# Kernel optimization log

Measured on AMD Instinct MI355X. Metric: run time of the kernel, lower is better.

## Reference

```python
import jax, jax.numpy as jnp
import numpy as np
from jax import lax

B0, H0, W0, C0, NH0 = 8, 128, 128, 192, 6
SPLIT = (8, 16)
BN_EPS = 1e-5


def setup_inputs() -> dict:
    key = jax.random.key(0)
    ks = jax.random.split(key, 32)
    r = lambda i, shape, s=0.02: jax.random.normal(ks[i], shape, dtype=jnp.float32) * s
    C, C8 = C0, C0 // 8
    L = H0 * W0
    return dict(
        x=jax.random.normal(ks[0], (B0, L, C), dtype=jnp.float32),
        w_qkv=r(1, (C, 3 * C)), b_qkv=r(2, (3 * C,)),
        w_dw1=r(3, (C, 1, 3, 3), 0.1), b_dw1=r(4, (C,)),
        g_bn1=1.0 + r(5, (C,)), be_bn1=r(6, (C,)),
        w_si1=r(7, (C8, C), 0.05), b_si1=r(8, (C8,)),
        g_si=1.0 + r(9, (C8,)), be_si=r(10, (C8,)),
        w_si2=r(11, (1, C8), 0.05), b_si2=r(12, (1,)),
        w_ci1=r(13, (C8, C), 0.05), b_ci1=r(14, (C8,)),
        g_ci=1.0 + r(15, (C8,)), be_ci=r(16, (C8,)),
        w_ci2=r(17, (C, C8), 0.05), b_ci2=r(18, (C,)),
        w_dw2=r(19, (C, 1, 3, 3), 0.1), b_dw2=r(20, (C,)),
        g_bn2=1.0 + r(21, (C,)), be_bn2=r(22, (C,)),
        w_proj=r(23, (C, C)), b_proj=r(24, (C,)),
        H=H0, W=W0,
    )


def _bn(x, g, b):  # eval-mode BatchNorm2d, running_mean=0, running_var=1, NCHW
    return x * (g / jnp.sqrt(1.0 + BN_EPS))[:, None, None] + b[:, None, None]


def _gelu(x):
    return jax.nn.gelu(x, approximate=False)  # torch nn.GELU default (erf)


def _dwconv3x3(x, w, b):  # x:(B,C,H,W), w:(C,1,3,3) depthwise
    y = lax.conv_general_dilated(x, w, (1, 1), 'SAME',
                                 feature_group_count=x.shape[1],
                                 dimension_numbers=('NCHW', 'OIHW', 'NCHW'))
    return y + b[:, None, None]


def _c1x1(x, w, b):  # 1x1 conv, w:(O,C)
    return jnp.einsum('bchw,oc->bohw', x, w) + b[:, None, None]


def _win_attn(q, k, v, H, W, Hs, Ws, nh):
    # q,k,v: (B, H*W, Cb). qkv1==qkv2==qkv3 in the source (same Linear on same x),
    # so attn1+attn2+attn3 == 3*attn1 and v1+v2+v3 == 3*v1 (faithful math).
    B, L, Cb = q.shape
    hd = Cb // nh
    scale = hd ** (-0.5)
    T = Hs * Ws

    def to_win(t):  # (B,L,Cb) -> (nW, nh, T, hd)
        t = t.reshape(B, H // Hs, Hs, W // Ws, Ws, Cb)
        t = t.transpose(0, 1, 3, 2, 4, 5).reshape(-1, T, nh, hd)
        return t.transpose(0, 2, 1, 3)

    qw, kw, vw = to_win(q), to_win(k), to_win(v)
    attn = jnp.einsum('wntd,wnsd->wnts', qw, kw) * (3.0 * scale)
    attn = jax.nn.softmax(attn, axis=-1)
    out = jnp.einsum('wnts,wnsd->wntd', attn, 3.0 * vw)  # (nW, nh, T, hd)
    out = out.transpose(0, 2, 1, 3).reshape(-1, T, Cb)
    out = out.reshape(B, H // Hs, W // Ws, Hs, Ws, Cb)
    out = out.transpose(0, 1, 3, 2, 4, 5).reshape(B, H, W, Cb)
    return out


def _forward(x, w_qkv, b_qkv, w_dw1, b_dw1, g_bn1, be_bn1,
             w_si1, b_si1, g_si, be_si, w_si2, b_si2,
             w_ci1, b_ci1, g_ci, be_ci, w_ci2, b_ci2,
             w_dw2, b_dw2, g_bn2, be_bn2, w_proj, b_proj, H, W):
    B, L, C = x.shape
    Ch = C // 2
    nh = NH0 // 2

    qkv = (x @ w_qkv + b_qkv).reshape(B, L, 3, C).transpose(2, 0, 1, 3)  # (3,B,L,C)
    mx = max(SPLIT)
    pad_b = (mx - H % mx) % mx
    pad_r = (mx - W % mx) % mx
    qi = qkv.reshape(3 * B, H, W, C)
    qi = jnp.pad(qi, ((0, 0), (0, pad_b), (0, pad_r), (0, 0)))
    _H, _W = H + pad_b, W + pad_r
    qkv = qi.reshape(3, B, _H * _W, C)
    q, k, v = qkv[0], qkv[1], qkv[2]

    fu1 = _win_attn(q[..., :Ch], k[..., :Ch], v[..., :Ch], _H, _W, SPLIT[0], SPLIT[1], nh)
    fu2 = _win_attn(q[..., Ch:], k[..., Ch:], v[..., Ch:], _H, _W, SPLIT[1], SPLIT[0], nh)
    fu = jnp.concatenate([fu1[:, :H, :W, :].reshape(B, L, Ch),
                          fu2[:, :H, :W, :].reshape(B, L, Ch)], axis=-1)

    # NOTE: the source does x.reshape(B,C,L) (a raw reshape, NOT a transpose) -- replicated.
    x_img = x.reshape(B, C, H, W)
    conv_x1 = _gelu(_bn(_dwconv3x3(x_img, w_dw1, b_dw1), g_bn1, be_bn1))

    s = _c1x1(conv_x1, w_si1, b_si1)
    s = _c1x1(_gelu(_bn(s, g_si, be_si)), w_si2, b_si2)   # (B,1,H,W)
    spatial_map = s.reshape(B, L, 1)

    c = conv_x1.mean(axis=(2, 3), keepdims=True)           # AdaptiveAvgPool2d(1)
    c = _c1x1(c, w_ci1, b_ci1)
    c = _c1x1(_gelu(_bn(c, g_ci, be_ci)), w_ci2, b_ci2)    # (B,C,1,1)
    channel_map = c.reshape(B, 1, C)

    fu = fu + fu * jax.nn.sigmoid(spatial_map)
    fu_img = jnp.swapaxes(fu, -2, -1).reshape(B, C, H, W)
    fu_img = _gelu(_bn(_dwconv3x3(fu_img, w_dw2, b_dw2), g_bn2, be_bn2))
    fu = fu_img.transpose(0, 2, 3, 1).reshape(B, L, C)
    fu = fu + fu * jax.nn.sigmoid(channel_map)
    return fu @ w_proj + b_proj


def reference(x, w_qkv, b_qkv, w_dw1, b_dw1, g_bn1, be_bn1,
              w_si1, b_si1, g_si, be_si, w_si2, b_si2,
              w_ci1, b_ci1, g_ci, be_ci, w_ci2, b_ci2,
              w_dw2, b_dw2, g_bn2, be_bn2, w_proj, b_proj, H, W):
    return _forward(x, w_qkv, b_qkv, w_dw1, b_dw1, g_bn1, be_bn1,
                    w_si1, b_si1, g_si, be_si, w_si2, b_si2,
                    w_ci1, b_ci1, g_ci, be_ci, w_ci2, b_ci2,
                    w_dw2, b_dw2, g_bn2, be_bn2, w_proj, b_proj, H, W)
```

## Files before the change

### kernel.cpp

```cpp
#include <hip/hip_runtime.h>

#define Bn 8
#define Hn 128
#define Wn 128
#define Cn 192
#define Ln (Hn*Wn)
#define Mn (Bn*Ln)
#define FUn ((size_t)Mn*Cn)
#define BANKn ((size_t)Mn*96)
#define BN_RSQ 0.9999950000374997f

typedef unsigned short ushort_t;
typedef __attribute__((ext_vector_type(8))) short short8;
typedef __attribute__((ext_vector_type(4))) float f32x4;
typedef __attribute__((ext_vector_type(4))) unsigned int uint4v;

static __device__ __forceinline__ float gelu_f(float x) {
    return 0.5f * x * (1.0f + erff(x * 0.7071067811865475f));
}
static __device__ __forceinline__ float gate1p(float x) {
    return 1.0f + 1.0f / (1.0f + __expf(-x));
}
static __device__ __forceinline__ unsigned short f2bf(float f) {
    unsigned u = __float_as_uint(f);
    return (unsigned short)((u + 0x7FFFu + ((u >> 16) & 1u)) >> 16);
}
static __device__ __forceinline__ unsigned int pk2(float lo, float hi) {
    return (unsigned int)f2bf(lo) | ((unsigned int)f2bf(hi) << 16);
}
static __device__ __forceinline__ float bf2f(ushort_t u) {
    return __uint_as_float((unsigned)u << 16);
}

__global__ __launch_bounds__(256) void qkv_mfma(const ushort_t* __restrict__ Ab,
        const float* __restrict__ Bw, const float* __restrict__ bias,
        ushort_t* __restrict__ Qp, ushort_t* __restrict__ Kp,
        ushort_t* __restrict__ Vp)
{
    __shared__ __align__(16) ushort_t As[128 * 64];
    __shared__ __align__(16) ushort_t Bs[96 * 64];
    const int m0 = blockIdx.y * 128;
    const int n0g = blockIdx.x * 96;
    const int part = n0g / 192;
    const int coln = n0g - part * 192;
    ushort_t* dst = part == 0 ? Qp : (part == 1 ? Kp : Vp);
    ushort_t* bptr = dst + (coln ? BANKn : 0);
    const int tid = threadIdx.x;
    const int lane = tid & 63;
    const int wrow = (tid >> 6) * 32;
    const int r0 = lane >> 4, cl = lane & 15;
    f32x4 acc[2][6] = {};

    for (int ks = 0; ks < 3; ++ks) {
        const int k0 = ks * 64;
        if (ks) __syncthreads();
        #pragma unroll
        for (int i = 0; i < 2; ++i) {
            int s = tid + i * 256;
            int row = s >> 2, q = s & 3;
            const ushort_t* src = Ab + (size_t)(m0 + row) * 192 + k0 + q * 16;
            uint4 u0 = *(const uint4*)(src);
            uint4 u1 = *(const uint4*)(src + 8);
            int r7 = row & 7;
            *(uint4*)&As[row * 64 + (((q * 2) ^ r7) * 8)] = u0;
            *(uint4*)&As[row * 64 + (((q * 2 + 1) ^ r7) * 8)] = u1;
        }
        #pragma unroll
        for (int i = 0; i < 3; ++i) {
            int f = tid + i * 256;
            int col = f % 96, kslot = f / 96;
            uint4v wv;
            #pragma unroll
            for (int e2 = 0; e2 < 4; ++e2) {
                float lo = Bw[(size_t)(k0 + kslot * 8 + 2 * e2)     * 576 + n0g + col];
                float hi = Bw[(size_t)(k0 + kslot * 8 + 2 * e2 + 1) * 576 + n0g + col];
                wv[e2] = pk2(lo, hi);
            }
            *(uint4v*)&Bs[col * 64 + ((kslot ^ (col & 7)) * 8)] = wv;
        }
        __syncthreads();
        #pragma unroll
        for (int kk = 0; kk < 2; ++kk) {
            int kslot = kk * 4 + r0;
            int ra0 = wrow + cl, ra1 = wrow + 16 + cl;
            short8 a0 = *(const short8*)&As[ra0 * 64 + ((kslot ^ (ra0 & 7)) * 8)];
            short8 a1 = *(const short8*)&As[ra1 * 64 + ((kslot ^ (ra1 & 7)) * 8)];
            #pragma unroll
            for (int n = 0; n < 6; ++n) {
                int col = n * 16 + cl;
                short8 bn = *(const short8*)&Bs[col * 64 + ((kslot ^ (col & 7)) * 8)];
                acc[0][n] = __builtin_amdgcn_mfma_f32_16x16x32_bf16(a0, bn, acc[0][n], 0, 0, 0);
                acc[1][n] = __builtin_amdgcn_mfma_f32_16x16x32_bf16(a1, bn, acc[1][n], 0, 0, 0);
            }
        }
    }
    float bv[6];
    #pragma unroll
    for (int n = 0; n < 6; ++n) bv[n] = bias[n0g + n * 16 + cl];
    #pragma unroll
    for (int m = 0; m < 2; ++m) {
        #pragma unroll
        for (int j = 0; j < 4; ++j) {
            int row = m0 + wrow + m * 16 + r0 * 4 + j;
            int b = row >> 14, l = row & 16383;
            int h = l >> 7, w = l & 127;
            int win, t;
            if (coln == 0) { win = (h >> 3) * 8 + (w >> 4);  t = (h & 7) * 16 + (w & 15); }
            else           { win = (h >> 4) * 16 + (w >> 3); t = (h & 15) * 8 + (w & 7); }
            size_t wb3 = (size_t)(b * 128 + win) * 3;
            #pragma unroll
            for (int n = 0; n < 6; ++n) {
                int col96 = n * 16 + cl;
                int head = col96 >> 5, ch = col96 & 31;
                size_t off = (wb3 + head) * 4096 +
                             (part == 2 ? ch * 128 + t : t * 32 + ch);
                bptr[off] = f2bf(acc[m][n][j] + bv[n]);
            }
        }
    }
}

__global__ __launch_bounds__(256) void proj_mfma(const ushort_t* __restrict__ Ab,
        const float* __restrict__ Bw, const float* __restrict__ bias,
        float* __restrict__ Cout)
{
    __shared__ __align__(16) ushort_t As[128 * 64];
    __shared__ __align__(16) ushort_t Bs[96 * 64];
    const int m0 = blockIdx.x * 128;
    const int n0 = blockIdx.y * 96;
    const int tid = threadIdx.x;
    const int lane = tid & 63;
    const int wrow = (tid >> 6) * 32;
    const int r0 = lane >> 4, cl = lane & 15;
    f32x4 acc[2][6] = {};

    for (int ks = 0; ks < 3; ++ks) {
        const int k0 = ks * 64;
        if (ks) __syncthreads();
        #pragma unroll
        for (int i = 0; i < 2; ++i) {
            int s = tid + i * 256;
            int row = s >> 2, q = s & 3;
            const ushort_t* src = Ab + (size_t)(m0 + row) * 192 + k0 + q * 16;
            uint4 u0 = *(const uint4*)(src);
            uint4 u1 = *(const uint4*)(src + 8);
            int r7 = row & 7;
            *(uint4*)&As[row * 64 + (((q * 2) ^ r7) * 8)] = u0;
            *(uint4*)&As[row * 64 + (((q * 2 + 1) ^ r7) * 8)] = u1;
        }
        #pragma unroll
        for (int i = 0; i < 3; ++i) {
            int f = tid + i * 256;
            int col = f % 96, kslot = f / 96;
            uint4v wv;
            #pragma unroll
            for (int e2 = 0; e2 < 4; ++e2) {
                float lo = Bw[(size_t)(k0 + kslot * 8 + 2 * e2)     * 192 + n0 + col];
                float hi = Bw[(size_t)(k0 + kslot * 8 + 2 * e2 + 1) * 192 + n0 + col];
                wv[e2] = pk2(lo, hi);
            }
            *(uint4v*)&Bs[col * 64 + ((kslot ^ (col & 7)) * 8)] = wv;
        }
        __syncthreads();
        #pragma unroll
        for (int kk = 0; kk < 2; ++kk) {
            int kslot = kk * 4 + r0;
            int ra0 = wrow + cl, ra1 = wrow + 16 + cl;
            short8 a0 = *(const short8*)&As[ra0 * 64 + ((kslot ^ (ra0 & 7)) * 8)];
            short8 a1 = *(const short8*)&As[ra1 * 64 + ((kslot ^ (ra1 & 7)) * 8)];
            #pragma unroll
            for (int n = 0; n < 6; ++n) {
                int col = n * 16 + cl;
                short8 bn = *(const short8*)&Bs[col * 64 + ((kslot ^ (col & 7)) * 8)];
                acc[0][n] = __builtin_amdgcn_mfma_f32_16x16x32_bf16(a0, bn, acc[0][n], 0, 0, 0);
                acc[1][n] = __builtin_amdgcn_mfma_f32_16x16x32_bf16(a1, bn, acc[1][n], 0, 0, 0);
            }
        }
    }
    #pragma unroll
    for (int m = 0; m < 2; ++m) {
        #pragma unroll
        for (int n = 0; n < 6; ++n) {
            int col = n0 + n * 16 + cl;
            float bv = bias[col];
            #pragma unroll
            for (int j = 0; j < 4; ++j) {
                int row = m0 + wrow + m * 16 + r0 * 4 + j;
                Cout[(size_t)row * 192 + col] = acc[m][n][j] + bv;
            }
        }
    }
}

__global__ __launch_bounds__(256) void attn_mfma(const ushort_t* __restrict__ Qp,
        const ushort_t* __restrict__ Kp, const ushort_t* __restrict__ Vp,
        const float* __restrict__ gate_s, ushort_t* __restrict__ fu_b)
{
    const int widx = threadIdx.x >> 6;
    const int idx = blockIdx.x * 4 + widx;
    const int jhalf = idx & 1;
    const int sub0 = idx >> 1;
    const int branch = (sub0 >= 3072) ? 1 : 0;
    const int sub = sub0 - branch * 3072;
    const int head = sub >> 10;
    const int b = (sub >> 7) & 7;
    const int win = sub & 127;
    const int L = threadIdx.x & 63;
    const int g = L >> 4, q = L & 15;
    int hb, wb;
    if (branch == 0) { hb = (win >> 3) * 8;  wb = (win & 7) * 16; }
    else             { hb = (win >> 4) * 16; wb = (win & 15) * 8; }
    const int cf = branch * 96 + head * 32;
    const int jbase = jhalf * 4;

    const size_t base = (branch ? BANKn : 0)
                      + ((size_t)(b * 128 + win) * 3 + head) * 4096;
    const ushort_t* Qw = Qp + base;
    const ushort_t* Kw = Kp + base;
    const ushort_t* Vw = Vp + base;

    short8 kf[8], qf[4];
    #pragma unroll
    for (int i = 0; i < 8; ++i)
        kf[i] = *(const short8*)(Kw + (16 * i + q) * 32 + 8 * g);
    #pragma unroll
    for (int jj = 0; jj < 4; ++jj)
        qf[jj] = *(const short8*)(Qw + (16 * (jbase + jj) + q) * 32 + 8 * g);
    short8 vf[2][4];
    #pragma unroll
    for (int dblk = 0; dblk < 2; ++dblk)
        #pragma unroll
        for (int s = 0; s < 4; ++s)
            vf[dblk][s] = *(const short8*)(Vw + (16 * dblk + q) * 128 + 32 * s + 8 * g);

    const float SC = 0.5303300858899106f;
    const int src0 = q + ((g & 1) << 5);
    const bool thi = (g >> 1) != 0;
    const bool glo = (g < 2);
    #pragma unroll
    for (int jj = 0; jj < 4; ++jj) {
        const int j = jbase + jj;
        unsigned wA[8], wB[8];
        float ss = 0.0f;
        #pragma unroll
        for (int i = 0; i < 8; ++i) {
            f32x4 z = {};
            f32x4 S = __builtin_amdgcn_mfma_f32_16x16x32_bf16(kf[i], qf[jj], z, 0, 0, 0);
            float p0 = __expf(S[0] * SC), p1 = __expf(S[1] * SC);
            float p2 = __expf(S[2] * SC), p3 = __expf(S[3] * SC);
            ss += (p0 + p1) + (p2 + p3);
            wA[i] = pk2(p0, p1);
            wB[i] = pk2(p2, p3);
        }
        ss += __shfl_xor(ss, 16);
        ss += __shfl_xor(ss, 32);
        int l_own;
        if (branch == 0) l_own = (hb + j) * Wn + wb + q;
        else             l_own = (hb + 2 * j + (q >> 3)) * Wn + wb + (q & 7);
        float s_own = 3.0f * gate_s[(size_t)b * Ln + l_own] / ss;

        f32x4 O0 = {}, O1 = {};
        #pragma unroll
        for (int s = 0; s < 4; ++s) {
            unsigned a0  = (unsigned)__shfl((int)wA[2*s],     src0);
            unsigned b0  = (unsigned)__shfl((int)wB[2*s],     src0);
            unsigned a0h = (unsigned)__shfl((int)wA[2*s],     src0 + 16);
            unsigned b0h = (unsigned)__shfl((int)wB[2*s],     src0 + 16);
            unsigned a1  = (unsigned)__shfl((int)wA[2*s+1],   src0);
            unsigned b1  = (unsigned)__shfl((int)wB[2*s+1],   src0);
            unsigned a1h = (unsigned)__shfl((int)wA[2*s+1],   src0 + 16);
            unsigned b1h = (unsigned)__shfl((int)wB[2*s+1],   src0 + 16);
            uint4v B2u;
            B2u[0] = thi ? a1  : a0;
            B2u[1] = thi ? b1  : b0;
            B2u[2] = thi ? a1h : a0h;
            B2u[3] = thi ? b1h : b0h;
            short8 B2 = *(short8*)&B2u;
            O0 = __builtin_amdgcn_mfma_f32_16x16x32_bf16(vf[0][s], B2, O0, 0, 0, 0);
            O1 = __builtin_amdgcn_mfma_f32_16x16x32_bf16(vf[1][s], B2, O1, 0, 0, 0);
        }
        unsigned w0 = pk2(O0[0] * s_own, O0[1] * s_own);
        unsigned w1 = pk2(O0[2] * s_own, O0[3] * s_own);
        unsigned w2 = pk2(O1[0] * s_own, O1[1] * s_own);
        unsigned w3 = pk2(O1[2] * s_own, O1[3] * s_own);
        unsigned a0 = (unsigned)__shfl((int)w0, src0);
        unsigned a1 = (unsigned)__shfl((int)w1, src0);
        unsigned b0 = (unsigned)__shfl((int)w0, src0 + 16);
        unsigned b1 = (unsigned)__shfl((int)w1, src0 + 16);
        unsigned c0 = (unsigned)__shfl((int)w2, src0);
        unsigned c1 = (unsigned)__shfl((int)w3, src0);
        unsigned d0 = (unsigned)__shfl((int)w2, src0 + 16);
        unsigned d1 = (unsigned)__shfl((int)w3, src0 + 16);
        uint4 o = make_uint4(glo ? a0 : c0, glo ? a1 : c1,
                             glo ? b0 : d0, glo ? b1 : d1);
        *(uint4*)(fu_b + (size_t)(b * Ln + l_own) * 192 + cf + 8 * g) = o;
    }
}

__global__ __launch_bounds__(256) void conv1_k(const float* __restrict__ x,
        const float* __restrict__ wdw, const float* __restrict__ bdw,
        const float* __restrict__ g1, const float* __restrict__ be1,
        ushort_t* __restrict__ conv1b, ushort_t* __restrict__ xb,
        float* __restrict__ pooled16)
{
    int bc = blockIdx.x;
    int rg = blockIdx.y;
    int c = bc % 192;
    const float* plane = x + (size_t)bc * Ln;
    int t = threadIdx.x;
    int sx = t & 31, sy = t >> 5;
    int w0 = sx * 4, h = rg * 8 + sy;
    float wk[9];
    #pragma unroll
    for (int i = 0; i < 9; ++i) wk[i] = wdw[c * 9 + i];
    float gb = g1[c] * BN_RSQ, bb = be1[c], bd = bdw[c];

    float a[3][6];
    #pragma unroll
    for (int i = 0; i < 3; ++i) {
        int hh = h - 1 + i;
        float4 m = make_float4(0.f, 0.f, 0.f, 0.f);
        if (hh >= 0 && hh < Hn)
            m = *(const float4*)(plane + hh * Wn + w0);
        float lf = __shfl_up(m.w, 1);
        float rt = __shfl_down(m.x, 1);
        a[i][0] = sx ? lf : 0.0f;
        a[i][1] = m.x; a[i][2] = m.y; a[i][3] = m.z; a[i][4] = m.w;
        a[i][5] = (sx < 31) ? rt : 0.0f;
    }
    *(uint2*)(xb + (size_t)bc * Ln + h * Wn + w0) =
        make_uint2(pk2(a[1][1], a[1][2]), pk2(a[1][3], a[1][4]));
    float psum = 0.0f;
    float o[4];
    #pragma unroll
    for (int p = 0; p < 4; ++p) {
        float s = wk[0] * a[0][p];
        s = fmaf(wk[1], a[0][p + 1], s);
        s = fmaf(wk[2], a[0][p + 2], s);
        s = fmaf(wk[3], a[1][p],     s);
        s = fmaf(wk[4], a[1][p + 1], s);
        s = fmaf(wk[5], a[1][p + 2], s);
        s = fmaf(wk[6], a[2][p],     s);
        s = fmaf(wk[7], a[2][p + 1], s);
        s = fmaf(wk[8], a[2][p + 2], s);
        float y = gelu_f((s + bd) * gb + bb);
        psum += y;
        o[p] = y;
    }
    *(uint2*)(conv1b + (size_t)bc * Ln + h * Wn + w0) =
        make_uint2(pk2(o[0], o[1]), pk2(o[2], o[3]));
    __shared__ float red[4];
    for (int off = 32; off; off >>= 1) psum += __shfl_down(psum, off);
    if ((t & 63) == 0) red[t >> 6] = psum;
    __syncthreads();
    if (t == 0)
        pooled16[bc * 16 + rg] = red[0] + red[1] + red[2] + red[3];
}

__global__ __launch_bounds__(128) void spatial_gate_k(const ushort_t* __restrict__ conv1b,
        const float* __restrict__ ws1g, const float* __restrict__ bs1,
        const float* __restrict__ gsi, const float* __restrict__ besi,
        const float* __restrict__ ws2, const float* __restrict__ bs2,
        float* __restrict__ gate_s)
{
    int bh = blockIdx.x;
    int b = bh >> 7, h = bh & 127;
    int w = threadIdx.x;
    __shared__ float ws1T[192 * 24];
    for (int i = w; i < 192 * 24; i += 128) {
        int c = i / 24, o = i - c * 24;
        ws1T[i] = ws1g[o * 192 + c];
    }
    __syncthreads();
    float acc24[24] = {};
    const ushort_t* base = conv1b + (size_t)b * 192 * Ln + h * Wn + w;
    #pragma unroll 4
    for (int c = 0; c < 192; ++c) {
        float v = bf2f(base[(size_t)c * Ln]);
        const float4* wp = (const float4*)&ws1T[c * 24];
        #pragma unroll
        for (int o4 = 0; o4 < 6; ++o4) {
            float4 wv = wp[o4];
            acc24[o4*4+0] = fmaf(v, wv.x, acc24[o4*4+0]);
            acc24[o4*4+1] = fmaf(v, wv.y, acc24[o4*4+1]);
            acc24[o4*4+2] = fmaf(v, wv.z, acc24[o4*4+2]);
            acc24[o4*4+3] = fmaf(v, wv.w, acc24[o4*4+3]);
        }
    }
    float s2 = bs2[0];
    #pragma unroll
    for (int o = 0; o < 24; ++o)
        s2 = fmaf(gelu_f((acc24[o] + bs1[o]) * (gsi[o] * BN_RSQ) + besi[o]), ws2[o], s2);
    gate_s[(size_t)bh * 128 + w] = gate1p(s2);
}

__global__ __launch_bounds__(192) void channel_gate_k(const float* __restrict__ pooled16,
        const float* __restrict__ w1, const float* __restrict__ b1,
        const float* __restrict__ g, const float* __restrict__ be,
        const float* __restrict__ w2, const float* __restrict__ b2,
        float* __restrict__ gate_c)
{
    int b = blockIdx.x, t = threadIdx.x;
    __shared__ float pl[192];
    __shared__ float h1[24];
    int bc = b * 192 + t;
    float s = 0.0f;
    #pragma unroll
    for (int i = 0; i < 16; ++i) s += pooled16[bc * 16 + i];
    pl[t] = s * (1.0f / Ln);
    __syncthreads();
    if (t < 24) {
        float a = b1[t];
        for (int c = 0; c < 192; ++c) a = fmaf(pl[c], w1[t * 192 + c], a);
        a = a * (g[t] * BN_RSQ) + be[t];
        h1[t] = gelu_f(a);
    }
    __syncthreads();
    float a = b2[t];
    #pragma unroll
    for (int o = 0; o < 24; ++o) a = fmaf(h1[o], w2[t * 24 + o], a);
    gate_c[b * 192 + t] = gate1p(a);
}

__global__ __launch_bounds__(256) void dwconv2_k(const ushort_t* __restrict__ fu_b,
        const float* __restrict__ gate_c,
        const float* __restrict__ wdw, const float* __restrict__ bdw,
        const float* __restrict__ g2, const float* __restrict__ be2,
        ushort_t* __restrict__ out2b)
{
    int bh = blockIdx.x >> 1;
    int whalf = blockIdx.x & 1;
    int b = bh >> 7, h = bh & 127;
    int tid = threadIdx.x;
    __shared__ float cwp[24 * 105];
    for (int idx = tid; idx < 24 * 96; idx += 256) {
        int c8 = idx / 96, r = idx - c8 * 96;
        float v;
        if (r < 72) {
            int i = r / 9, p = r - i * 9;
            v = wdw[(c8 * 8 + i) * 9 + p];
        } else {
            int r2 = r - 72;
            int i = r2 / 3, j = r2 - i * 3;
            int c = c8 * 8 + i;
            float A = g2[c] * BN_RSQ;
            v = (j == 0) ? A : (j == 1) ? fmaf(bdw[c], A, be2[c])
                                        : gate_c[b * 192 + c];
        }
        cwp[c8 * 105 + r] = v;
    }
    __syncthreads();
    const size_t outrow = (size_t)(b * Ln + h * Wn) * 192;
    for (int it = 0; it < 6; ++it) {
        int item = it * 256 + tid;
        int w = whalf * 64 + item / 24;
        int c8 = item % 24;
        int co = c8 * 8;
        const float* wp = &cwp[c8 * 105];
        uint4 nb[3][3];
        #pragma unroll
        for (int r = 0; r < 3; ++r)
            #pragma unroll
            for (int d = 0; d < 3; ++d)
                nb[r][d] = make_uint4(0u, 0u, 0u, 0u);
        #pragma unroll
        for (int r = 0; r < 3; ++r) {
            int hh = h - 1 + r;
            if (hh < 0 || hh >= Hn) continue;
            const ushort_t* rp = fu_b + (size_t)(b * Ln + hh * Wn) * 192 + co;
            #pragma unroll
            for (int d = 0; d < 3; ++d) {
                int w2 = w - 1 + d;
                if (w2 < 0 || w2 >= Wn) continue;
                nb[r][d] = *(const uint4*)(rp + (size_t)w2 * 192);
            }
        }
        unsigned ou[4];
        #pragma unroll
        for (int i = 0; i < 8; ++i) {
            float s = 0.0f;
            #pragma unroll
            for (int r = 0; r < 3; ++r) {
                #pragma unroll
                for (int d = 0; d < 3; ++d) {
                    unsigned word = ((const unsigned*)&nb[r][d])[i >> 1];
                    float v = __uint_as_float((i & 1) ? (word & 0xffff0000u)
                                                      : (word << 16));
                    s = fmaf(wp[i * 9 + r * 3 + d], v, s);
                }
            }
            float A = wp[72 + i * 3];
            float Bc = wp[72 + i * 3 + 1];
            float G = wp[72 + i * 3 + 2];
            float y = gelu_f(fmaf(s, A, Bc)) * G;
            if (i & 1) ou[i >> 1] |= (unsigned)f2bf(y) << 16;
            else       ou[i >> 1] = (unsigned)f2bf(y);
        }
        *(uint4*)(out2b + outrow + (size_t)w * 192 + co) =
            make_uint4(ou[0], ou[1], ou[2], ou[3]);
    }
}

extern "C" void kernel_launch(void* const* d_in, const int* in_sizes, int n_in,
                              void* d_out, int out_size, void* d_ws, size_t ws_size,
                              hipStream_t stream) {
    (void)in_sizes; (void)n_in; (void)out_size; (void)ws_size;
    const float* x      = (const float*)d_in[0];
    const float* w_qkv  = (const float*)d_in[1];
    const float* b_qkv  = (const float*)d_in[2];
    const float* w_dw1  = (const float*)d_in[3];
    const float* b_dw1  = (const float*)d_in[4];
    const float* g_bn1  = (const float*)d_in[5];
    const float* be_bn1 = (const float*)d_in[6];
    const float* w_si1  = (const float*)d_in[7];
    const float* b_si1  = (const float*)d_in[8];
    const float* g_si   = (const float*)d_in[9];
    const float* be_si  = (const float*)d_in[10];
    const float* w_si2  = (const float*)d_in[11];
    const float* b_si2  = (const float*)d_in[12];
    const float* w_ci1  = (const float*)d_in[13];
    const float* b_ci1  = (const float*)d_in[14];
    const float* g_ci   = (const float*)d_in[15];
    const float* be_ci  = (const float*)d_in[16];
    const float* w_ci2  = (const float*)d_in[17];
    const float* b_ci2  = (const float*)d_in[18];
    const float* w_dw2  = (const float*)d_in[19];
    const float* b_dw2  = (const float*)d_in[20];
    const float* g_bn2  = (const float*)d_in[21];
    const float* be_bn2 = (const float*)d_in[22];
    const float* w_proj = (const float*)d_in[23];
    const float* b_proj = (const float*)d_in[24];

    float* ws = (float*)d_ws;
    ushort_t* conv1b = (ushort_t*)ws;
    ushort_t* Qp     = (ushort_t*)ws;
    ushort_t* Kp     = (ushort_t*)(ws + FUn / 2);
    ushort_t* out2b  = (ushort_t*)(ws + 8000000);
    float* gate_s    = ws + FUn;
    float* gate_c    = gate_s + (size_t)Bn * Ln;
    float* pooled16  = gate_c + Bn * 192;
    ushort_t* xb     = (ushort_t*)d_out;
    ushort_t* fu_b   = (ushort_t*)d_out;
    ushort_t* Vp     = (ushort_t*)d_out + FUn;

    conv1_k<<<dim3(Bn * 192, 16), 256, 0, stream>>>(x, w_dw1, b_dw1, g_bn1, be_bn1,
                                                    conv1b, xb, pooled16);
    spatial_gate_k<<<Bn * Hn, 128, 0, stream>>>(conv1b, w_si1, b_si1, g_si, be_si,
                                                w_si2, b_si2, gate_s);
    channel_gate_k<<<Bn, 192, 0, stream>>>(pooled16, w_ci1, b_ci1, g_ci, be_ci,
                                           w_ci2, b_ci2, gate_c);
    qkv_mfma<<<dim3(6, Mn / 128), 256, 0, stream>>>(xb, w_qkv, b_qkv, Qp, Kp, Vp);
    attn_mfma<<<3072, 256, 0, stream>>>(Qp, Kp, Vp, gate_s, fu_b);
    dwconv2_k<<<Bn * Hn * 2, 256, 0, stream>>>(fu_b, gate_c,
                                               w_dw2, b_dw2, g_bn2, be_bn2, out2b);
    proj_mfma<<<dim3(Mn / 128, 2), 256, 0, stream>>>(out2b, w_proj, b_proj, (float*)d_out);
}
```

Measured before the change: 340.4 us.

## Tile QKV GEMM rows by attention window and stage outputs through LDS

Each QKV GEMM block now processes the 128 tokens of one attention window instead of 128 contiguous rows, gathering input rows by window geometry. The output tile is staged in shared memory, transposed for V, and written out as 16-byte vector stores into the windowed Q/K/V layouts. This replaces the earlier scattered 2-byte stores. In exchange it adds extra barriers, LDS traffic, and strided input row reads.

```diff
diff --git a/kernel.cpp b/kernel.cpp
--- a/kernel.cpp
+++ b/kernel.cpp
@@ -37,14 +37,21 @@
         ushort_t* __restrict__ Qp, ushort_t* __restrict__ Kp,
         ushort_t* __restrict__ Vp)
 {
-    __shared__ __align__(16) ushort_t As[128 * 64];
-    __shared__ __align__(16) ushort_t Bs[96 * 64];
-    const int m0 = blockIdx.y * 128;
-    const int n0g = blockIdx.x * 96;
-    const int part = n0g / 192;
-    const int coln = n0g - part * 192;
-    ushort_t* dst = part == 0 ? Qp : (part == 1 ? Kp : Vp);
-    ushort_t* bptr = dst + (coln ? BANKn : 0);
+    __shared__ __align__(16) ushort_t smem[128 * 64 + 96 * 64];
+    ushort_t* As = smem;
+    ushort_t* Bs = smem + 128 * 64;
+    ushort_t* St = smem;
+    ushort_t* Stv = smem;
+    const int br = blockIdx.x & 1;
+    const int partp = blockIdx.x >> 1;
+    const int wid = blockIdx.y;
+    const int b = wid >> 7, win = wid & 127;
+    const int n0g = partp * 192 + br * 96;
+    ushort_t* dst = partp == 0 ? Qp : (partp == 1 ? Kp : Vp);
+    ushort_t* bptr = dst + (br ? BANKn : 0);
+    int hb, wb;
+    if (br == 0) { hb = (win >> 3) * 8;  wb = (win & 7) * 16; }
+    else         { hb = (win >> 4) * 16; wb = (win & 15) * 8; }
     const int tid = threadIdx.x;
     const int lane = tid & 63;
     const int wrow = (tid >> 6) * 32;
@@ -58,7 +65,9 @@
         for (int i = 0; i < 2; ++i) {
             int s = tid + i * 256;
             int row = s >> 2, q = s & 3;
-            const ushort_t* src = Ab + (size_t)(m0 + row) * 192 + k0 + q * 16;
+            int l = (br == 0) ? (hb + (row >> 4)) * Wn + wb + (row & 15)
+                              : (hb + (row >> 3)) * Wn + wb + (row & 7);
+            const ushort_t* src = Ab + (size_t)(b * Ln + l) * 192 + k0 + q * 16;
             uint4 u0 = *(const uint4*)(src);
             uint4 u1 = *(const uint4*)(src + 8);
             int r7 = row & 7;
@@ -97,25 +106,43 @@
     float bv[6];
     #pragma unroll
     for (int n = 0; n < 6; ++n) bv[n] = bias[n0g + n * 16 + cl];
-    #pragma unroll
-    for (int m = 0; m < 2; ++m) {
-        #pragma unroll
-        for (int j = 0; j < 4; ++j) {
-            int row = m0 + wrow + m * 16 + r0 * 4 + j;
-            int b = row >> 14, l = row & 16383;
-            int h = l >> 7, w = l & 127;
-            int win, t;
-            if (coln == 0) { win = (h >> 3) * 8 + (w >> 4);  t = (h & 7) * 16 + (w & 15); }
-            else           { win = (h >> 4) * 16 + (w >> 3); t = (h & 15) * 8 + (w & 7); }
-            size_t wb3 = (size_t)(b * 128 + win) * 3;
-            #pragma unroll
-            for (int n = 0; n < 6; ++n) {
-                int col96 = n * 16 + cl;
-                int head = col96 >> 5, ch = col96 & 31;
-                size_t off = (wb3 + head) * 4096 +
-                             (part == 2 ? ch * 128 + t : t * 32 + ch);
-                bptr[off] = f2bf(acc[m][n][j] + bv[n]);
-            }
+    __syncthreads();
+    const size_t hbase = (size_t)wid * 3;
+    if (partp < 2) {
+        #pragma unroll
+        for (int m = 0; m < 2; ++m)
+            #pragma unroll
+            for (int n = 0; n < 6; ++n)
+                #pragma unroll
+                for (int j = 0; j < 4; ++j) {
+                    int t = wrow + m * 16 + r0 * 4 + j;
+                    St[t * 104 + n * 16 + cl] = f2bf(acc[m][n][j] + bv[n]);
+                }
+        __syncthreads();
+        #pragma unroll
+        for (int i = 0; i < 6; ++i) {
+            int f = tid + i * 256;
+            int ch8 = f & 3, t = (f >> 2) & 127, hd = f >> 9;
+            uint4 v = *(const uint4*)&St[t * 104 + hd * 32 + ch8 * 8];
+            *(uint4*)(bptr + (hbase + hd) * 4096 + t * 32 + ch8 * 8) = v;
+        }
+    } else {
+        #pragma unroll
+        for (int m = 0; m < 2; ++m)
+            #pragma unroll
+            for (int n = 0; n < 6; ++n)
+                #pragma unroll
+                for (int j = 0; j < 4; ++j) {
+                    int t = wrow + m * 16 + r0 * 4 + j;
+                    Stv[(n * 16 + cl) * 136 + t] = f2bf(acc[m][n][j] + bv[n]);
+                }
+        __syncthreads();
+        #pragma unroll
+        for (int i = 0; i < 6; ++i) {
+            int f = tid + i * 256;
+            int t16 = f & 15, ch = (f >> 4) & 31, hd = f >> 9;
+            uint4 v = *(const uint4*)&Stv[(hd * 32 + ch) * 136 + t16 * 8];
+            *(uint4*)(bptr + (hbase + hd) * 4096 + ch * 128 + t16 * 8) = v;
         }
     }
 }
@@ -549,7 +576,7 @@
                                                 w_si2, b_si2, gate_s);
     channel_gate_k<<<Bn, 192, 0, stream>>>(pooled16, w_ci1, b_ci1, g_ci, be_ci,
                                            w_ci2, b_ci2, gate_c);
-    qkv_mfma<<<dim3(6, Mn / 128), 256, 0, stream>>>(xb, w_qkv, b_qkv, Qp, Kp, Vp);
+    qkv_mfma<<<dim3(6, Bn * 128), 256, 0, stream>>>(xb, w_qkv, b_qkv, Qp, Kp, Vp);
     attn_mfma<<<3072, 256, 0, stream>>>(Qp, Kp, Vp, gate_s, fu_b);
     dwconv2_k<<<Bn * Hn * 2, 256, 0, stream>>>(fu_b, gate_c,
                                                w_dw2, b_dw2, g_bn2, be_bn2, out2b);
```

New measurement: 293.2 us. 13.9% less time.
